# Performance work log

Hardware: AMD Instinct MI355X
Metric: run time of the kernel (lower is better)

## Reference

```python
import jax, jax.numpy as jnp
import numpy as np

D_STATE = 16
D_CONV = 4
DT_RANK = 16  # ceil(d_model/16) = ceil(256/16)
N_LAYERS = 2
EPS = 1e-5


def _layernorm(x, g, b):
    m = jnp.mean(x, -1, keepdims=True)
    v = jnp.var(x, -1, keepdims=True)
    return (x - m) * jax.lax.rsqrt(v + EPS) * g + b


def _causal_conv(x, w, b):
    # x [B,L,D], depthwise causal conv, w [D,K], b [D]
    K = w.shape[1]
    L = x.shape[1]
    xp = jnp.pad(x, ((0, 0), (K - 1, 0), (0, 0)))
    y = sum(xp[:, k:k + L, :] * w[:, k] for k in range(K))
    return y + b


def _selective_scan(u, dt, A, Bm, Cm, D_skip):
    # u, dt [B,L,d]; A [d,n]; Bm, Cm [B,L,n]; D_skip [d]
    def step(h, inp):
        dt_t, B_t, C_t, u_t = inp  # [B,d],[B,n],[B,n],[B,d]
        dA = jnp.exp(dt_t[:, :, None] * A)                      # [B,d,n]
        h = dA * h + dt_t[:, :, None] * B_t[:, None, :] * u_t[:, :, None]
        y = jnp.einsum('bdn,bn->bd', h, C_t)
        return h, y

    Bsz, L, d = u.shape
    h0 = jnp.zeros((Bsz, d, A.shape[1]), u.dtype)
    xs = (dt.transpose(1, 0, 2), Bm.transpose(1, 0, 2),
          Cm.transpose(1, 0, 2), u.transpose(1, 0, 2))
    _, ys = jax.lax.scan(step, h0, xs)                          # [L,B,d]
    return ys.transpose(1, 0, 2) + u * D_skip


def _mamba_block(x, Wip, cw, cb, Wxp, Wdt, bdt, Alog, Dp, Wout):
    xz = x @ Wip                                                # [B,L,2*d_inner]
    d_inner = Wip.shape[1] // 2
    xc, z = xz[..., :d_inner], xz[..., d_inner:]
    xc = jax.nn.silu(_causal_conv(xc, cw, cb))
    xdbl = xc @ Wxp                                             # [B,L,dt_rank+2n]
    dt = jax.nn.softplus(xdbl[..., :DT_RANK] @ Wdt + bdt)
    Bm = xdbl[..., DT_RANK:DT_RANK + D_STATE]
    Cm = xdbl[..., DT_RANK + D_STATE:]
    A = -jnp.exp(Alog)
    y = _selective_scan(xc, dt, A, Bm, Cm, Dp)
    y = y * jax.nn.silu(z)
    return y @ Wout


def reference(z_t, W_in, b_in, ln_g, ln_b, W_inproj, conv_w, conv_b, W_xproj,
              W_dt, b_dt, A_log, D_skip, W_out, W_outp, b_outp, lno_g, lno_b):
    x = z_t @ W_in + b_in                                       # [B,L,d_model]
    for i in range(N_LAYERS):
        res = x
        xn = _layernorm(x, ln_g[i], ln_b[i])
        x = res + _mamba_block(xn, W_inproj[i], conv_w[i], conv_b[i],
                               W_xproj[i], W_dt[i], b_dt[i], A_log[i],
                               D_skip[i], W_out[i])  # dropout is identity in eval
    u = x @ W_outp + b_outp
    return _layernorm(u, lno_g, lno_b)


def setup_inputs() -> dict:
    key = jax.random.key(0)
    B, L = 16, 2048
    d_input, d_model, d_output, d_inner = 1088, 256, 64, 512
    n = N_LAYERS
    ks = jax.random.split(key, 10)

    def rn(k, shape, fan):
        return jax.random.normal(k, shape, jnp.float32) / np.float32(np.sqrt(fan))

    A_init = jnp.log(jnp.arange(1, D_STATE + 1, dtype=jnp.float32))
    return {
        'z_t': jax.random.normal(ks[0], (B, L, d_input), jnp.float32),
        'W_in': rn(ks[1], (d_input, d_model), d_input),
        'b_in': jnp.zeros((d_model,), jnp.float32),
        'ln_g': jnp.ones((n, d_model), jnp.float32),
        'ln_b': jnp.zeros((n, d_model), jnp.float32),
        'W_inproj': rn(ks[2], (n, d_model, 2 * d_inner), d_model),
        'conv_w': rn(ks[3], (n, d_inner, D_CONV), D_CONV),
        'conv_b': jnp.zeros((n, d_inner), jnp.float32),
        'W_xproj': rn(ks[4], (n, d_inner, DT_RANK + 2 * D_STATE), d_inner),
        'W_dt': rn(ks[5], (n, DT_RANK, d_inner), DT_RANK),
        'b_dt': jnp.full((n, d_inner), -4.6, jnp.float32),  # softplus ~ 0.01
        'A_log': jnp.broadcast_to(A_init, (n, d_inner, D_STATE)) + 0.0,
        'D_skip': jnp.ones((n, d_inner), jnp.float32),
        'W_out': rn(ks[6], (n, d_inner, d_model), d_inner),
        'W_outp': rn(ks[7], (d_model, d_output), d_model),
        'b_outp': jnp.zeros((d_output,), jnp.float32),
        'lno_g': jnp.ones((d_output,), jnp.float32),
        'lno_b': jnp.zeros((d_output,), jnp.float32),
    }
```

## Files before the change

### kernel.cpp

```cpp
#include <hip/hip_runtime.h>
#include <hip/hip_bf16.h>
#include <math.h>
#include <stdint.h>

#define L_SEQ 2048
#define BATCH 16
#define NROWS (BATCH * L_SEQ)
#define DMODEL 256
#define DINNER 512
#define C_CH 32
#define T_CH 64
#define LOG2E 1.4426950408889634f

typedef __attribute__((ext_vector_type(8))) __bf16 bf16x8;
typedef __attribute__((ext_vector_type(4))) float f32x4;
typedef __attribute__((ext_vector_type(8))) unsigned short u16x8;
typedef __attribute__((address_space(1))) const uint32_t gu32;
typedef __attribute__((address_space(3))) uint32_t lu32;

#if __has_builtin(__builtin_amdgcn_exp2f)
#define EXP2F __builtin_amdgcn_exp2f
#else
#define EXP2F exp2f
#endif

__device__ __forceinline__ float sigmoidf_(float x) { return 1.f / (1.f + __expf(-x)); }

__device__ __forceinline__ unsigned short f2bf(float f) {
    union { float f; uint32_t u; } v; v.f = f;
    uint32_t r = v.u + 0x7FFF + ((v.u >> 16) & 1);
    return (unsigned short)(r >> 16);
}
__device__ __forceinline__ float bf2f(unsigned short h) {
    union { uint32_t u; float f; } v; v.u = ((uint32_t)h) << 16;
    return v.f;
}

__device__ __forceinline__ void gld16(const void* g, void* l) {
    __builtin_amdgcn_global_load_lds((gu32*)g, (lu32*)l, 16, 0, 0);
}

template <int N> __device__ __forceinline__ void waitv() {
    if constexpr (N == 0)      asm volatile("s_waitcnt vmcnt(0)" ::: "memory");
    else if constexpr (N == 3) asm volatile("s_waitcnt vmcnt(3)" ::: "memory");
    else if constexpr (N == 4) asm volatile("s_waitcnt vmcnt(4)" ::: "memory");
    else if constexpr (N == 6) asm volatile("s_waitcnt vmcnt(6)" ::: "memory");
    else if constexpr (N == 8) asm volatile("s_waitcnt vmcnt(8)" ::: "memory");
}

__global__ __launch_bounds__(256) void wtrans(const float* __restrict__ W,
                                              unsigned short* __restrict__ Wt, int K, int N) {
    int idx = blockIdx.x * 256 + threadIdx.x;
    if (idx < K * N) {
        int n = idx / K, k = idx % K;
        Wt[idx] = f2bf(W[(size_t)k * N + n]);
    }
}
__global__ __launch_bounds__(256) void wtrans_pad(const float* __restrict__ W,
                                                  unsigned short* __restrict__ Wt,
                                                  int K, int Nreal, int Npad) {
    int idx = blockIdx.x * 256 + threadIdx.x;
    if (idx < Npad * K) {
        int n = idx / K, k = idx % K;
        Wt[idx] = (n < Nreal) ? f2bf(W[(size_t)k * Nreal + n]) : (unsigned short)0;
    }
}

template <int TM, int BK, bool A_F32, bool HAS_BIAS, bool HAS_RES, bool OUT_BF16>
__global__ __launch_bounds__(256) void gemm_bf16(
    const void* __restrict__ Aptr, const unsigned short* __restrict__ Bt,
    const float* __restrict__ bias, const float* __restrict__ res,
    void* __restrict__ Cout, int M, int N, int K, int Nout)
{
    constexpr int MR = TM / 32;
    constexpr int EWA = A_F32 ? 4 : 2;
    constexpr int RBA = BK * EWA;
    constexpr int RBB = BK * 2;
    constexpr int ABYTES = TM * RBA;
    constexpr int BBYTES = 128 * RBB;
    constexpr int OPSA = ABYTES / 4096;
    constexpr int OPSB = BBYTES / 4096;
    constexpr int VOPS = OPSA + OPSB;
    constexpr bool SWZA = (RBA >= 128);
    constexpr bool SWZB = (RBB >= 128);
    constexpr int KK = BK / 32;
    __shared__ __align__(16) char Alds[2][ABYTES];
    __shared__ __align__(16) char Blds[2][BBYTES];
    const int tid = threadIdx.x;
    const int w = tid >> 6, lane = tid & 63;

    const int nwg = gridDim.x;
    const int q = nwg >> 3;
    const int wg = (blockIdx.x & 7) * q + (blockIdx.x >> 3);
    const int nx = N >> 7;
    const int bm = (wg / nx) * TM, bn = (wg % nx) * 128;

    const int wr = (w >> 1) * (TM / 2), wc = (w & 1) * 64;
    const int fr = lane & 15, fq = lane >> 4;
    const size_t KbB = (size_t)K * 2;
    const size_t KbA = (size_t)K * EWA;

    const char* Ab = (const char*)Aptr;
    const char* Bb = (const char*)Bt;
    const int lds0 = w * 1024;

    f32x4 acc[MR][4];
#pragma unroll
    for (int m = 0; m < MR; m++)
#pragma unroll
        for (int n = 0; n < 4; n++) acc[m][n] = (f32x4){0.f, 0.f, 0.f, 0.f};

    auto stageA = [&](int buf, int k0) {
        char* lA = Alds[buf];
#pragma unroll
        for (int i = 0; i < OPSA; i++) {
            const int o = i * 4096 + tid * 16;
            const int row = o / RBA;
            int col = o % RBA;
            if constexpr (SWZA) col ^= (row & 7) << 4;
            gld16(Ab + (size_t)(bm + row) * KbA + (size_t)k0 * EWA + col,
                  lA + i * 4096 + lds0);
        }
    };
    auto stageB = [&](int buf, int k0) {
        char* lB = Blds[buf];
#pragma unroll
        for (int i = 0; i < OPSB; i++) {
            const int o = i * 4096 + tid * 16;
            const int row = o / RBB;
            int col = o % RBB;
            if constexpr (SWZB) col ^= (row & 7) << 4;
            gld16(Bb + (size_t)(bn + row) * KbB + (size_t)k0 * 2 + col,
                  lB + i * 4096 + lds0);
        }
    };
    auto compute = [&](int buf) {
        bf16x8 af[MR][KK], bg[4][KK];
        const char* lA = Alds[buf];
        const char* lB = Blds[buf];
#pragma unroll
        for (int m = 0; m < MR; m++) {
            const int row = wr + m * 16 + fr;
            const int sw = SWZA ? ((row & 7) << 4) : 0;
#pragma unroll
            for (int kk = 0; kk < KK; kk++) {
                if constexpr (A_F32) {
                    const int b0 = row * RBA + kk * 128 + fq * 32;
                    float4 x0 = *(const float4*)(lA + (b0 ^ sw));
                    float4 x1 = *(const float4*)(lA + ((b0 + 16) ^ sw));
                    bf16x8 a;
                    a[0]=(__bf16)x0.x; a[1]=(__bf16)x0.y; a[2]=(__bf16)x0.z; a[3]=(__bf16)x0.w;
                    a[4]=(__bf16)x1.x; a[5]=(__bf16)x1.y; a[6]=(__bf16)x1.z; a[7]=(__bf16)x1.w;
                    af[m][kk] = a;
                } else {
                    const int c = kk * 64 + fq * 16;
                    af[m][kk] = *(const bf16x8*)(lA + row * RBA + (c ^ sw));
                }
            }
        }
#pragma unroll
        for (int n = 0; n < 4; n++) {
            const int row = wc + n * 16 + fr;
            const int sw = SWZB ? ((row & 7) << 4) : 0;
#pragma unroll
            for (int kk = 0; kk < KK; kk++) {
                const int c = kk * 64 + fq * 16;
                bg[n][kk] = *(const bf16x8*)(lB + row * RBB + (c ^ sw));
            }
        }
#pragma unroll
        for (int kk = 0; kk < KK; kk++)
#pragma unroll
            for (int m = 0; m < MR; m++)
#pragma unroll
                for (int n = 0; n < 4; n++)
                    acc[m][n] = __builtin_amdgcn_mfma_f32_16x16x32_bf16(af[m][kk], bg[n][kk], acc[m][n], 0, 0, 0);
    };

    const int NT = K / BK;

    stageA(0, 0); stageB(0, 0);
    asm volatile("s_waitcnt vmcnt(0) lgkmcnt(0)" ::: "memory");
    __builtin_amdgcn_s_barrier();
    __builtin_amdgcn_sched_barrier(0);

    for (int kt = 0; kt < NT; ++kt) {
        const int cur = kt & 1;
        const bool has_next = (kt + 1 < NT);
        if (has_next) {
            const int k0 = (kt + 1) * BK;
            stageA(cur ^ 1, k0); stageB(cur ^ 1, k0);
            waitv<VOPS>();
        } else {
            waitv<0>();
        }
        __builtin_amdgcn_s_barrier();
        __builtin_amdgcn_sched_barrier(0);

        compute(cur);

        asm volatile("s_waitcnt lgkmcnt(0)" ::: "memory");
        __builtin_amdgcn_s_barrier();
        __builtin_amdgcn_sched_barrier(0);
    }

#pragma unroll
    for (int m = 0; m < MR; m++) {
#pragma unroll
        for (int n = 0; n < 4; n++) {
            int col = bn + wc + n * 16 + fr;
            if (col < Nout) {
#pragma unroll
                for (int r = 0; r < 4; r++) {
                    int row = bm + wr + m * 16 + fq * 4 + r;
                    float v = acc[m][n][r];
                    if (HAS_BIAS) v += bias[col];
                    if (HAS_RES)  v += res[(size_t)row * Nout + col];
                    if (OUT_BF16) ((unsigned short*)Cout)[(size_t)row * Nout + col] = f2bf(v);
                    else          ((float*)Cout)[(size_t)row * Nout + col] = v;
                }
            }
        }
    }
}

__global__ __launch_bounds__(256) void ln256(
    const float* __restrict__ x, const float* __restrict__ g,
    const float* __restrict__ b, unsigned short* __restrict__ out)
{
    int lane = threadIdx.x & 63, wid = threadIdx.x >> 6;
    size_t r = (size_t)blockIdx.x * 4 + wid;
    const float4 v = *(const float4*)&x[r * 256 + lane * 4];
    float s = v.x + v.y + v.z + v.w;
    float sq = v.x * v.x + v.y * v.y + v.z * v.z + v.w * v.w;
#pragma unroll
    for (int off = 32; off; off >>= 1) { s += __shfl_xor(s, off); sq += __shfl_xor(sq, off); }
    float mean = s * (1.f / 256.f);
    float var = sq * (1.f / 256.f) - mean * mean;
    float rs = rsqrtf(var + 1e-5f);
    float4 gv = *(const float4*)&g[lane * 4];
    float4 bv = *(const float4*)&b[lane * 4];
    ushort4 o;
    o.x = f2bf((v.x - mean) * rs * gv.x + bv.x);
    o.y = f2bf((v.y - mean) * rs * gv.y + bv.y);
    o.z = f2bf((v.z - mean) * rs * gv.z + bv.z);
    o.w = f2bf((v.w - mean) * rs * gv.w + bv.w);
    *(ushort4*)&out[r * 256 + lane * 4] = o;
}

__global__ __launch_bounds__(256) void ln64(
    const float* __restrict__ t, const float* __restrict__ g,
    const float* __restrict__ b, float* __restrict__ out)
{
    int lane = threadIdx.x & 63, wid = threadIdx.x >> 6;
    size_t r = (size_t)blockIdx.x * 4 + wid;
    float v = t[r * 64 + lane];
    float s = v, sq = v * v;
#pragma unroll
    for (int off = 32; off; off >>= 1) { s += __shfl_xor(s, off); sq += __shfl_xor(sq, off); }
    float mean = s * (1.f / 64.f);
    float var = sq * (1.f / 64.f) - mean * mean;
    out[r * 64 + lane] = (v - mean) * rsqrtf(var + 1e-5f) * g[lane] + b[lane];
}

__global__ __launch_bounds__(256) void conv_silu8(
    const unsigned short* __restrict__ xz, const float* __restrict__ w,
    const float* __restrict__ cb, unsigned short* __restrict__ xc)
{
    int idx = blockIdx.x * 256 + threadIdx.x;
    int d8 = (idx & 63) << 3;
    int l  = (idx >> 6) & 2047;
    int b  = idx >> 17;
    const unsigned short* base = xz + ((size_t)b * L_SEQ + l) * 1024 + d8;
    u16x8 t0 = {0,0,0,0,0,0,0,0}, t1 = t0, t2 = t0;
    u16x8 t3 = *(const u16x8*)base;
    if (l >= 1) t2 = *(const u16x8*)(base - 1024);
    if (l >= 2) t1 = *(const u16x8*)(base - 2048);
    if (l >= 3) t0 = *(const u16x8*)(base - 3072);
    u16x8 o;
#pragma unroll
    for (int j = 0; j < 8; j++) {
        float4 wv = *(const float4*)&w[(d8 + j) * 4];
        float acc = cb[d8 + j];
        acc = fmaf(bf2f(t0[j]), wv.x, acc);
        acc = fmaf(bf2f(t1[j]), wv.y, acc);
        acc = fmaf(bf2f(t2[j]), wv.z, acc);
        acc = fmaf(bf2f(t3[j]), wv.w, acc);
        o[j] = f2bf(acc * sigmoidf_(acc));
    }
    *(u16x8*)&xc[((size_t)b * L_SEQ + l) * 512 + d8] = o;
}

__global__ __launch_bounds__(256) void scan_pass1(
    const unsigned short* __restrict__ xc, const float* __restrict__ xdbl,
    const float* __restrict__ Wdt, const float* __restrict__ bdt,
    const float* __restrict__ Alog,
    float* __restrict__ Tbuf, float* __restrict__ Sbuf)
{
    __shared__ float xs[T_CH][32];
    int idx = blockIdx.x * 256 + threadIdx.x;
    int d = idx & 511;
    int c = (idx >> 9) & (C_CH - 1);
    int b = idx >> 14;
    size_t r0 = (size_t)b * L_SEQ + (size_t)c * T_CH;
#pragma unroll
    for (int ii = 0; ii < 2; ii++) {
        int i = threadIdx.x + ii * 256, row = i >> 3, qq = i & 7;
        *(float4*)&xs[row][qq * 4] = *(const float4*)&xdbl[(r0 + row) * 48 + qq * 4];
    }
    __syncthreads();

    float wdt[16];
#pragma unroll
    for (int j = 0; j < 16; j++) wdt[j] = Wdt[j * 512 + d];
    const float bd = bdt[d];

    float a[16], a2[16], S[16];
#pragma unroll
    for (int n = 0; n < 16; n++) a[n] = -__expf(Alog[d * 16 + n]);
#pragma unroll
    for (int n = 0; n < 16; n++) a2[n] = a[n] * LOG2E;
#pragma unroll
    for (int n = 0; n < 16; n++) S[n] = 0.f;
    bool pow_ok = true;
#pragma unroll
    for (int n = 1; n < 16; n++)
        pow_ok = pow_ok && (fabsf(a[n] - (n + 1) * a[0]) <= 1e-3f * (n + 1) * fabsf(a[0]));
    const float a0l2 = a[0] * LOG2E;
    float Tsum = 0.f;

    if (pow_ok) {
        for (int t = 0; t < T_CH; t++) {
            float dtr = bd;
#pragma unroll
            for (int j = 0; j < 16; j++) dtr = fmaf(xs[t][j], wdt[j], dtr);
            float dtv = (dtr > 20.f) ? dtr : __logf(1.f + __expf(dtr));
            float u = bf2f(xc[(r0 + t) * 512 + d]);
            float dtu = dtv * u;
            Tsum += dtv;
            float e1 = EXP2F(dtv * a0l2), e2 = e1 * e1;
            S[0] = fmaf(e1, S[0], dtu * xs[t][16]);
            S[1] = fmaf(e2, S[1], dtu * xs[t][17]);
            float pm2 = e1, pm1 = e2;
#pragma unroll
            for (int n = 2; n < 16; n++) {
                float cur = pm2 * e2;
                S[n] = fmaf(cur, S[n], dtu * xs[t][16 + n]);
                pm2 = pm1; pm1 = cur;
            }
        }
    } else {
        for (int t = 0; t < T_CH; t++) {
            float dtr = bd;
#pragma unroll
            for (int j = 0; j < 16; j++) dtr = fmaf(xs[t][j], wdt[j], dtr);
            float dtv = (dtr > 20.f) ? dtr : __logf(1.f + __expf(dtr));
            float u = bf2f(xc[(r0 + t) * 512 + d]);
            float dtu = dtv * u;
            Tsum += dtv;
#pragma unroll
            for (int n = 0; n < 16; n++) {
                float dA = EXP2F(dtv * a2[n]);
                S[n] = fmaf(dA, S[n], dtu * xs[t][16 + n]);
            }
        }
    }
    Tbuf[idx] = Tsum;
    size_t o = (size_t)idx * 16;
#pragma unroll
    for (int qq = 0; qq < 4; qq++)
        *(float4*)&Sbuf[o + qq * 4] = make_float4(S[qq*4], S[qq*4+1], S[qq*4+2], S[qq*4+3]);
}

__global__ __launch_bounds__(256) void scan_pass2(
    const float* __restrict__ Tbuf, const float* __restrict__ Alog,
    float* __restrict__ Sbuf)
{
    int g = blockIdx.x * 256 + threadIdx.x;
    int nd = g & 8191;
    int b = g >> 13;
    int d = nd >> 4, n = nd & 15;
    const float a2 = -__expf(Alog[d * 16 + n]) * LOG2E;
    float H = 0.f;
    for (int c = 0; c < C_CH; c++) {
        size_t base = (size_t)(b * C_CH + c);
        float T = Tbuf[base * 512 + d];
        float P = EXP2F(T * a2);
        size_t idx = base * 8192 + nd;
        float S = Sbuf[idx];
        float Hn = fmaf(P, H, S);
        Sbuf[idx] = H;
        H = Hn;
    }
}

__global__ __launch_bounds__(256) void scan_pass3(
    const unsigned short* __restrict__ xcin, const unsigned short* __restrict__ xz,
    const float* __restrict__ xdbl, const float* __restrict__ Wdt,
    const float* __restrict__ bdt, const float* __restrict__ Alog,
    const float* __restrict__ Dsk, const float* __restrict__ Sbuf,
    unsigned short* __restrict__ y)
{
    __shared__ float xs[T_CH][48];
    int idx = blockIdx.x * 256 + threadIdx.x;
    int d = idx & 511;
    int c = (idx >> 9) & (C_CH - 1);
    int b = idx >> 14;
    size_t r0 = (size_t)b * L_SEQ + (size_t)c * T_CH;
#pragma unroll
    for (int ii = 0; ii < 3; ii++) {
        int i = threadIdx.x + ii * 256, row = i / 12, qq = i % 12;
        *(float4*)&xs[row][qq * 4] = *(const float4*)&xdbl[(r0 + row) * 48 + qq * 4];
    }
    __syncthreads();

    float wdt[16];
#pragma unroll
    for (int j = 0; j < 16; j++) wdt[j] = Wdt[j * 512 + d];
    const float bd = bdt[d];

    float a[16], a2[16], h[16];
#pragma unroll
    for (int n = 0; n < 16; n++) a[n] = -__expf(Alog[d * 16 + n]);
#pragma unroll
    for (int n = 0; n < 16; n++) a2[n] = a[n] * LOG2E;
    {
        size_t o = (size_t)idx * 16;
#pragma unroll
        for (int qq = 0; qq < 4; qq++) {
            float4 v = *(const float4*)&Sbuf[o + qq * 4];
            h[qq*4] = v.x; h[qq*4+1] = v.y; h[qq*4+2] = v.z; h[qq*4+3] = v.w;
        }
    }
    bool pow_ok = true;
#pragma unroll
    for (int n = 1; n < 16; n++)
        pow_ok = pow_ok && (fabsf(a[n] - (n + 1) * a[0]) <= 1e-3f * (n + 1) * fabsf(a[0]));
    const float a0l2 = a[0] * LOG2E;
    const float Dv = Dsk[d];

    if (pow_ok) {
        for (int t = 0; t < T_CH; t++) {
            size_t ridx = (r0 + t) * 512 + d;
            float dtr = bd;
#pragma unroll
            for (int j = 0; j < 16; j++) dtr = fmaf(xs[t][j], wdt[j], dtr);
            float dtv = (dtr > 20.f) ? dtr : __logf(1.f + __expf(dtr));
            float u = bf2f(xcin[ridx]);
            float dtu = dtv * u;
            float e1 = EXP2F(dtv * a0l2), e2 = e1 * e1;
            float yv = 0.f;
            h[0] = fmaf(e1, h[0], dtu * xs[t][16]);  yv = fmaf(h[0], xs[t][32], yv);
            h[1] = fmaf(e2, h[1], dtu * xs[t][17]);  yv = fmaf(h[1], xs[t][33], yv);
            float pm2 = e1, pm1 = e2;
#pragma unroll
            for (int n = 2; n < 16; n++) {
                float cur = pm2 * e2;
                h[n] = fmaf(cur, h[n], dtu * xs[t][16 + n]);
                yv = fmaf(h[n], xs[t][32 + n], yv);
                pm2 = pm1; pm1 = cur;
            }
            yv = fmaf(u, Dv, yv);
            float z = bf2f(xz[(r0 + t) * 1024 + 512 + d]);
            y[ridx] = f2bf(yv * z * sigmoidf_(z));
        }
    } else {
        for (int t = 0; t < T_CH; t++) {
            size_t ridx = (r0 + t) * 512 + d;
            float dtr = bd;
#pragma unroll
            for (int j = 0; j < 16; j++) dtr = fmaf(xs[t][j], wdt[j], dtr);
            float dtv = (dtr > 20.f) ? dtr : __logf(1.f + __expf(dtr));
            float u = bf2f(xcin[ridx]);
            float dtu = dtv * u;
            float yv = 0.f;
#pragma unroll
            for (int n = 0; n < 16; n++) {
                float dA = EXP2F(dtv * a2[n]);
                h[n] = fmaf(dA, h[n], dtu * xs[t][16 + n]);
                yv = fmaf(h[n], xs[t][32 + n], yv);
            }
            yv = fmaf(u, Dv, yv);
            float z = bf2f(xz[(r0 + t) * 1024 + 512 + d]);
            y[ridx] = f2bf(yv * z * sigmoidf_(z));
        }
    }
}

extern "C" void kernel_launch(void* const* d_in, const int* in_sizes, int n_in,
                              void* d_out, int out_size, void* d_ws, size_t ws_size,
                              hipStream_t stream)
{
    const float* z_t     = (const float*)d_in[0];
    const float* W_in    = (const float*)d_in[1];
    const float* b_in    = (const float*)d_in[2];
    const float* ln_g    = (const float*)d_in[3];
    const float* ln_b    = (const float*)d_in[4];
    const float* W_inpr  = (const float*)d_in[5];
    const float* conv_w  = (const float*)d_in[6];
    const float* conv_b  = (const float*)d_in[7];
    const float* W_xproj = (const float*)d_in[8];
    const float* W_dt    = (const float*)d_in[9];
    const float* b_dt    = (const float*)d_in[10];
    const float* A_log   = (const float*)d_in[11];
    const float* D_skip  = (const float*)d_in[12];
    const float* W_out   = (const float*)d_in[13];
    const float* W_outp  = (const float*)d_in[14];
    const float* b_outp  = (const float*)d_in[15];
    const float* lno_g   = (const float*)d_in[16];
    const float* lno_b   = (const float*)d_in[17];
    float* out           = (float*)d_out;

    char* p = (char*)d_ws;
    float*          x    = (float*)p;          p += (size_t)NROWS * DMODEL * 4;
    unsigned short* xn   = (unsigned short*)p; p += (size_t)NROWS * DMODEL * 2;
    unsigned short* xc   = (unsigned short*)p; p += (size_t)NROWS * DINNER * 2;
    unsigned short* xz   = (unsigned short*)p; p += (size_t)NROWS * 1024 * 2;
    float*          xdbl = (float*)p;          p += (size_t)NROWS * 48 * 4;
    float*          Pregion = (float*)p;       p += (size_t)BATCH * C_CH * DINNER * 16 * 4;
    float*          Sbuf = (float*)p;          p += (size_t)BATCH * C_CH * DINNER * 16 * 4;
    unsigned short* WinT  = (unsigned short*)p; p += (size_t)256 * 1088 * 2;
    unsigned short* WipT  = (unsigned short*)p; p += (size_t)2 * 1024 * 256 * 2;
    unsigned short* WoutT = (unsigned short*)p; p += (size_t)2 * 256 * 512 * 2;
    unsigned short* WxpT  = (unsigned short*)p; p += (size_t)2 * 128 * 512 * 2;
    unsigned short* WopT  = (unsigned short*)p; p += (size_t)128 * 256 * 2;
    float* Tbuf = Pregion;
    float* otmp = Pregion;

    wtrans<<<(256 * 1088 + 255) / 256, 256, 0, stream>>>(W_in, WinT, 1088, 256);
    for (int l = 0; l < 2; l++) {
        wtrans<<<(1024 * 256 + 255) / 256, 256, 0, stream>>>(
            W_inpr + (size_t)l * 256 * 1024, WipT + (size_t)l * 1024 * 256, 256, 1024);
        wtrans<<<(256 * 512 + 255) / 256, 256, 0, stream>>>(
            W_out + (size_t)l * 512 * 256, WoutT + (size_t)l * 256 * 512, 512, 256);
        wtrans_pad<<<(128 * 512 + 255) / 256, 256, 0, stream>>>(
            W_xproj + (size_t)l * 512 * 48, WxpT + (size_t)l * 128 * 512, 512, 48, 128);
    }
    wtrans_pad<<<(128 * 256 + 255) / 256, 256, 0, stream>>>(W_outp, WopT, 256, 64, 128);

    gemm_bf16<64, 64, true, true, false, false><<<(NROWS / 64) * (256 / 128), 256, 0, stream>>>(
        z_t, WinT, b_in, nullptr, x, NROWS, 256, 1088, 256);

    for (int layer = 0; layer < 2; ++layer) {
        ln256<<<NROWS / 4, 256, 0, stream>>>(x, ln_g + layer * 256, ln_b + layer * 256, xn);
        gemm_bf16<128, 32, false, false, false, true><<<(NROWS / 128) * (1024 / 128), 256, 0, stream>>>(
            xn, WipT + (size_t)layer * 1024 * 256, nullptr, nullptr, xz, NROWS, 1024, 256, 1024);
        conv_silu8<<<NROWS * 64 / 256, 256, 0, stream>>>(
            xz, conv_w + layer * 512 * 4, conv_b + layer * 512, xc);
        gemm_bf16<64, 64, false, false, false, false><<<(NROWS / 64) * (128 / 128), 256, 0, stream>>>(
            xc, WxpT + (size_t)layer * 128 * 512, nullptr, nullptr, xdbl, NROWS, 128, 512, 48);

        const float* Al_l  = A_log + layer * 512 * 16;
        const float* Wdt_l = W_dt + layer * 16 * 512;
        const float* bdt_l = b_dt + layer * 512;
        scan_pass1<<<BATCH * C_CH * DINNER / 256, 256, 0, stream>>>(
            xc, xdbl, Wdt_l, bdt_l, Al_l, Tbuf, Sbuf);
        scan_pass2<<<BATCH * DINNER * 16 / 256, 256, 0, stream>>>(Tbuf, Al_l, Sbuf);
        scan_pass3<<<BATCH * C_CH * DINNER / 256, 256, 0, stream>>>(
            xc, xz, xdbl, Wdt_l, bdt_l, Al_l, D_skip + layer * 512, Sbuf, xc);

        if (layer == 0) {
            gemm_bf16<64, 64, false, false, true, false><<<(NROWS / 64) * (256 / 128), 256, 0, stream>>>(
                xc, WoutT, nullptr, x, x, NROWS, 256, 512, 256);
        } else {
            gemm_bf16<64, 64, false, false, true, true><<<(NROWS / 64) * (256 / 128), 256, 0, stream>>>(
                xc, WoutT + (size_t)256 * 512, nullptr, x, xn, NROWS, 256, 512, 256);
        }
    }

    gemm_bf16<64, 32, false, true, false, false><<<(NROWS / 64) * (128 / 128), 256, 0, stream>>>(
        xn, WopT, b_outp, nullptr, otmp, NROWS, 128, 256, 64);
    ln64<<<NROWS / 4, 256, 0, stream>>>(otmp, lno_g, lno_b, out);
}
```

Measured before the change: 549.2 us.

## Load GEMM B operand directly from global into registers, bypassing LDS

The B weight tile is no longer staged into a double-buffered LDS buffer. Each wave now reads its B fragments straight from global memory into registers at the start of every K step, and the vmcnt waits are adjusted to count those loads. This is meant to cut LDS traffic, LDS footprint and the swizzled LDS reads for B. The cost is that waves sharing the same columns load B redundantly, and the B loads are issued for the current step rather than prefetched, so global latency may be exposed before the MFMAs.

```diff
diff --git a/kernel.cpp b/kernel.cpp
--- a/kernel.cpp
+++ b/kernel.cpp
@@ -41,11 +41,13 @@
 }
 
 template <int N> __device__ __forceinline__ void waitv() {
-    if constexpr (N == 0)      asm volatile("s_waitcnt vmcnt(0)" ::: "memory");
-    else if constexpr (N == 3) asm volatile("s_waitcnt vmcnt(3)" ::: "memory");
-    else if constexpr (N == 4) asm volatile("s_waitcnt vmcnt(4)" ::: "memory");
-    else if constexpr (N == 6) asm volatile("s_waitcnt vmcnt(6)" ::: "memory");
-    else if constexpr (N == 8) asm volatile("s_waitcnt vmcnt(8)" ::: "memory");
+    if constexpr (N == 0)       asm volatile("s_waitcnt vmcnt(0)" ::: "memory");
+    else if constexpr (N == 4)  asm volatile("s_waitcnt vmcnt(4)" ::: "memory");
+    else if constexpr (N == 5)  asm volatile("s_waitcnt vmcnt(5)" ::: "memory");
+    else if constexpr (N == 6)  asm volatile("s_waitcnt vmcnt(6)" ::: "memory");
+    else if constexpr (N == 8)  asm volatile("s_waitcnt vmcnt(8)" ::: "memory");
+    else if constexpr (N == 10) asm volatile("s_waitcnt vmcnt(10)" ::: "memory");
+    else if constexpr (N == 12) asm volatile("s_waitcnt vmcnt(12)" ::: "memory");
 }
 
 __global__ __launch_bounds__(256) void wtrans(const float* __restrict__ W,
@@ -75,17 +77,12 @@
     constexpr int MR = TM / 32;
     constexpr int EWA = A_F32 ? 4 : 2;
     constexpr int RBA = BK * EWA;
-    constexpr int RBB = BK * 2;
     constexpr int ABYTES = TM * RBA;
-    constexpr int BBYTES = 128 * RBB;
     constexpr int OPSA = ABYTES / 4096;
-    constexpr int OPSB = BBYTES / 4096;
-    constexpr int VOPS = OPSA + OPSB;
+    constexpr int KK = BK / 32;
+    constexpr int BOPS = 4 * KK;
     constexpr bool SWZA = (RBA >= 128);
-    constexpr bool SWZB = (RBB >= 128);
-    constexpr int KK = BK / 32;
     __shared__ __align__(16) char Alds[2][ABYTES];
-    __shared__ __align__(16) char Blds[2][BBYTES];
     const int tid = threadIdx.x;
     const int w = tid >> 6, lane = tid & 63;
 
@@ -122,22 +119,19 @@
                   lA + i * 4096 + lds0);
         }
     };
-    auto stageB = [&](int buf, int k0) {
-        char* lB = Blds[buf];
-#pragma unroll
-        for (int i = 0; i < OPSB; i++) {
-            const int o = i * 4096 + tid * 16;
-            const int row = o / RBB;
-            int col = o % RBB;
-            if constexpr (SWZB) col ^= (row & 7) << 4;
-            gld16(Bb + (size_t)(bn + row) * KbB + (size_t)k0 * 2 + col,
-                  lB + i * 4096 + lds0);
+    auto loadB = [&](int k0, bf16x8 bg[4][KK]) {
+#pragma unroll
+        for (int n = 0; n < 4; n++) {
+            const int row = bn + wc + n * 16 + fr;
+            const char* bp = Bb + (size_t)row * KbB + (size_t)k0 * 2 + fq * 16;
+#pragma unroll
+            for (int kk = 0; kk < KK; kk++)
+                bg[n][kk] = *(const bf16x8*)(bp + kk * 64);
         }
     };
-    auto compute = [&](int buf) {
-        bf16x8 af[MR][KK], bg[4][KK];
+    auto compute = [&](int buf, bf16x8 bg[4][KK]) {
+        bf16x8 af[MR][KK];
         const char* lA = Alds[buf];
-        const char* lB = Blds[buf];
 #pragma unroll
         for (int m = 0; m < MR; m++) {
             const int row = wr + m * 16 + fr;
@@ -159,16 +153,6 @@
             }
         }
 #pragma unroll
-        for (int n = 0; n < 4; n++) {
-            const int row = wc + n * 16 + fr;
-            const int sw = SWZB ? ((row & 7) << 4) : 0;
-#pragma unroll
-            for (int kk = 0; kk < KK; kk++) {
-                const int c = kk * 64 + fq * 16;
-                bg[n][kk] = *(const bf16x8*)(lB + row * RBB + (c ^ sw));
-            }
-        }
-#pragma unroll
         for (int kk = 0; kk < KK; kk++)
 #pragma unroll
             for (int m = 0; m < MR; m++)
@@ -179,25 +163,22 @@
 
     const int NT = K / BK;
 
-    stageA(0, 0); stageB(0, 0);
-    asm volatile("s_waitcnt vmcnt(0) lgkmcnt(0)" ::: "memory");
-    __builtin_amdgcn_s_barrier();
-    __builtin_amdgcn_sched_barrier(0);
-
+    stageA(0, 0);
     for (int kt = 0; kt < NT; ++kt) {
         const int cur = kt & 1;
         const bool has_next = (kt + 1 < NT);
+        bf16x8 bg[4][KK];
+        loadB(kt * BK, bg);
         if (has_next) {
-            const int k0 = (kt + 1) * BK;
-            stageA(cur ^ 1, k0); stageB(cur ^ 1, k0);
-            waitv<VOPS>();
+            stageA(cur ^ 1, (kt + 1) * BK);
+            waitv<OPSA + BOPS>();
         } else {
-            waitv<0>();
+            waitv<BOPS>();
         }
         __builtin_amdgcn_s_barrier();
         __builtin_amdgcn_sched_barrier(0);
 
-        compute(cur);
+        compute(cur, bg);
 
         asm volatile("s_waitcnt lgkmcnt(0)" ::: "memory");
         __builtin_amdgcn_s_barrier();
```

Measured after the change: 645.9 us. +17.6%, slower.
